# Optimization experiments

Hardware: AMD Instinct MI355X
Metric: run time of the kernel (lower is better)

Reference implementation:

```python
import jax, jax.numpy as jnp
import numpy as np

N = 100000
E = 1600000
HID = 128
NODE_DIM = 128


def _sage_conv(h, src, dst, W_l, b_l, W_r, n_nodes):
    # PyG SAGEConv (mean aggr): out = lin_l(mean_{j in N(i)} h_j) + lin_r(h_i)
    msg = h[src]                                            # [E, d] gather
    s = jax.ops.segment_sum(msg, dst, num_segments=n_nodes)  # [N, d]
    cnt = jax.ops.segment_sum(jnp.ones((msg.shape[0], 1), h.dtype), dst,
                              num_segments=n_nodes)          # [N, 1]
    agg = jnp.where(cnt > 0, s / jnp.maximum(cnt, 1.0), 0.0)
    return agg @ W_l + b_l + h @ W_r


def setup_inputs() -> dict:
    key = jax.random.key(0)
    ks = jax.random.split(key, 12)
    sc = 0.05
    return {
        "pos": jax.random.normal(ks[0], (N, 3), jnp.float32),
        "atomic_number": jax.random.randint(ks[1], (N,), 0, 10, jnp.int64)
            if jax.config.jax_enable_x64 else jax.random.randint(ks[1], (N,), 0, 10, jnp.int32),
        "edge_index": jax.random.randint(ks[2], (2, E), 0, N, jnp.int32),
        # input_proj: Linear(4, HID) — stored as [in, out]
        "W_in": jax.random.normal(ks[3], (4, HID), jnp.float32) * sc,
        "b_in": jnp.zeros((HID,), jnp.float32),
        # conv1: SAGEConv(HID, HID): lin_l (bias), lin_r (no bias)
        "W1_l": jax.random.normal(ks[4], (HID, HID), jnp.float32) * sc,
        "b1": jnp.zeros((HID,), jnp.float32),
        "W1_r": jax.random.normal(ks[5], (HID, HID), jnp.float32) * sc,
        # conv2
        "W2_l": jax.random.normal(ks[6], (HID, HID), jnp.float32) * sc,
        "b2": jnp.zeros((HID,), jnp.float32),
        "W2_r": jax.random.normal(ks[7], (HID, HID), jnp.float32) * sc,
        # out: Linear(HID, NODE_DIM)
        "W_out": jax.random.normal(ks[8], (HID, NODE_DIM), jnp.float32) * sc,
        "b_out": jnp.zeros((NODE_DIM,), jnp.float32),
    }


def reference(pos, atomic_number, edge_index, W_in, b_in, W1_l, b1, W1_r,
              W2_l, b2, W2_r, W_out, b_out):
    src, dst = edge_index[0], edge_index[1]
    z_atom = (atomic_number.astype(pos.dtype) / 10.0)[:, None]   # [N, 1]
    x = jnp.concatenate([z_atom, pos], axis=-1)                   # [N, 4]
    h = jax.nn.relu(x @ W_in + b_in)
    h = jax.nn.relu(_sage_conv(h, src, dst, W1_l, b1, W1_r, h.shape[0]))
    h = jax.nn.relu(_sage_conv(h, src, dst, W2_l, b2, W2_r, h.shape[0]))
    node_states = h @ W_out + b_out                               # [N, node_dim]
    return node_states.mean(axis=0), node_states
```

## Files before the change

### kernel.cpp

```cpp
#include <hip/hip_runtime.h>

#define HID 128
#define BK_SHIFT 9
#define BK_NODES 512
#define BKCAP 10240
#define EDGES_PER_BLKA 8192

typedef _Float16 half_t;
typedef __attribute__((ext_vector_type(8))) _Float16 half8;
typedef __attribute__((ext_vector_type(4))) _Float16 half4;
typedef __attribute__((ext_vector_type(4))) float f32x4;

__global__ __launch_bounds__(256) void k_init(int* __restrict__ bcur,
                                              float* __restrict__ outmean) {
  int i = threadIdx.x;
  bcur[i] = i * BKCAP;
  if (i < HID) outmean[i] = 0.f;
}

__global__ __launch_bounds__(256) void k_packW5(const float* __restrict__ w0,
                                                const float* __restrict__ w1,
                                                const float* __restrict__ w2,
                                                const float* __restrict__ w3,
                                                const float* __restrict__ w4,
                                                half_t* __restrict__ o0,
                                                half_t* __restrict__ o1,
                                                half_t* __restrict__ o2,
                                                half_t* __restrict__ o3,
                                                half_t* __restrict__ o4) {
  int m = blockIdx.x >> 3;
  const float* W = (m == 0) ? w0 : (m == 1) ? w1 : (m == 2) ? w2 : (m == 3) ? w3 : w4;
  half_t* out = (m == 0) ? o0 : (m == 1) ? o1 : (m == 2) ? o2 : (m == 3) ? o3 : o4;
  int tid = (blockIdx.x & 7) * 256 + threadIdx.x;
  int lane = tid & 63;
  int frag = tid >> 6;
  int ks = frag >> 3, nt = frag & 7;
  int k0 = ks * 32 + ((lane >> 4) << 3);
  int col = nt * 16 + (lane & 15);
  half8 v;
#pragma unroll
  for (int i = 0; i < 8; ++i) v[i] = (half_t)W[(k0 + i) * HID + col];
  *(half8*)&out[(size_t)tid * 8] = v;
}

__global__ __launch_bounds__(256) void k_embed(const float* __restrict__ pos,
                                               const int* __restrict__ an,
                                               const float* __restrict__ Win,
                                               const float* __restrict__ bin,
                                               half_t* __restrict__ h, int n) {
  int t = blockIdx.x * 256 + threadIdx.x;
  int i = t >> 5, cg = t & 31;
  if (i >= n) return;
  int j0 = cg << 2;
  float z  = (float)an[i] / 10.0f;
  float px = pos[3 * i + 0], py = pos[3 * i + 1], pz = pos[3 * i + 2];
  float4 w0 = *(const float4*)&Win[0 * HID + j0];
  float4 w1 = *(const float4*)&Win[1 * HID + j0];
  float4 w2 = *(const float4*)&Win[2 * HID + j0];
  float4 w3 = *(const float4*)&Win[3 * HID + j0];
  float4 b  = *(const float4*)&bin[j0];
  float4 o;
  o.x = fmaxf(fmaf(z, w0.x, fmaf(px, w1.x, fmaf(py, w2.x, fmaf(pz, w3.x, b.x)))), 0.f);
  o.y = fmaxf(fmaf(z, w0.y, fmaf(px, w1.y, fmaf(py, w2.y, fmaf(pz, w3.y, b.y)))), 0.f);
  o.z = fmaxf(fmaf(z, w0.z, fmaf(px, w1.z, fmaf(py, w2.z, fmaf(pz, w3.z, b.z)))), 0.f);
  o.w = fmaxf(fmaf(z, w0.w, fmaf(px, w1.w, fmaf(py, w2.w, fmaf(pz, w3.w, b.w)))), 0.f);
  half4 ph;
  ph.x = (half_t)o.x; ph.y = (half_t)o.y; ph.z = (half_t)o.z; ph.w = (half_t)o.w;
  *(half4*)&h[(size_t)i * HID + j0] = ph;
}

__global__ __launch_bounds__(1024) void k_bucketA(const int* __restrict__ src,
                                                  const int* __restrict__ dst,
                                                  int* __restrict__ bcur,
                                                  unsigned* __restrict__ ebuf,
                                                  int e) {
  __shared__ int hist[256];
  __shared__ int resv[256];
  int t = threadIdx.x;
  if (t < 256) hist[t] = 0;
  __syncthreads();
  int e0 = blockIdx.x * EDGES_PER_BLKA;
  int myb[8], myr[8];
  unsigned mypk[8];
#pragma unroll
  for (int i = 0; i < 8; ++i) {
    int idx = e0 + i * 1024 + t;
    if (idx < e) {
      int d = dst[idx];
      int s = src[idx];
      int b = d >> BK_SHIFT;
      myb[i] = b;
      myr[i] = atomicAdd(&hist[b], 1);
      mypk[i] = ((unsigned)s << BK_SHIFT) | (unsigned)(d & (BK_NODES - 1));
    } else {
      myb[i] = -1;
    }
  }
  __syncthreads();
  if (t < 256) resv[t] = (hist[t] > 0) ? atomicAdd(&bcur[t], hist[t]) : 0;
  __syncthreads();
#pragma unroll
  for (int i = 0; i < 8; ++i) {
    if (myb[i] >= 0) ebuf[resv[myb[i]] + myr[i]] = mypk[i];
  }
}

__global__ __launch_bounds__(256) void k_bucketB(const unsigned* __restrict__ ebuf,
                                                 const int* __restrict__ bkend,
                                                 int* __restrict__ offs,
                                                 int* __restrict__ offsE,
                                                 int* __restrict__ csr, int n) {
  __shared__ int hist[BK_NODES];
  __shared__ int pscan[256];
  int b = blockIdx.x;
  int n0 = b << BK_SHIFT;
  int t = threadIdx.x;
  int ebeg = b * BKCAP, eend = bkend[b];
  hist[t] = 0; hist[t + 256] = 0;
  __syncthreads();
  for (int idx = ebeg + t; idx < eend; idx += 256) {
    atomicAdd(&hist[ebuf[idx] & (BK_NODES - 1)], 1);
  }
  __syncthreads();
  int h0 = hist[2 * t], h1 = hist[2 * t + 1];
  int ps = h0 + h1;
  pscan[t] = ps;
  __syncthreads();
  for (int d = 1; d < 256; d <<= 1) {
    int u = (t >= d) ? pscan[t - d] : 0;
    __syncthreads();
    pscan[t] += u;
    __syncthreads();
  }
  int base0 = ebeg + (pscan[t] - ps);
  int g0 = n0 + 2 * t, g1 = g0 + 1;
  if (g0 < n) { offs[g0] = base0;      offsE[g0] = base0 + h0; }
  if (g1 < n) { offs[g1] = base0 + h0; offsE[g1] = base0 + h0 + h1; }
  __syncthreads();
  hist[2 * t] = base0;
  hist[2 * t + 1] = base0 + h0;
  __syncthreads();
  for (int idx = ebeg + t; idx < eend; idx += 256) {
    unsigned pk = ebuf[idx];
    int dl = pk & (BK_NODES - 1);
    int slot = atomicAdd(&hist[dl], 1);
    csr[slot] = (int)(pk >> BK_SHIFT);
  }
}

__global__ __launch_bounds__(256) void k_aggmean_f16(const half_t* __restrict__ h,
                                                     const int* __restrict__ csr,
                                                     const int* __restrict__ offs,
                                                     const int* __restrict__ offsE,
                                                     half_t* __restrict__ out, int n) {
  int w = (blockIdx.x * 256 + threadIdx.x) >> 6;
  int lane = threadIdx.x & 63;
  if (w >= n) return;
  int cs = lane & 15, es = lane >> 4;
  int beg = offs[w], end = offsE[w];
  size_t coff = (size_t)(cs * 8);
  float acc[8];
#pragma unroll
  for (int j = 0; j < 8; ++j) acc[j] = 0.f;
  int e = beg;
  for (; e + 16 <= end; e += 16) {
    int s0 = csr[e + es];
    int s1 = csr[e + 4 + es];
    int s2 = csr[e + 8 + es];
    int s3 = csr[e + 12 + es];
    half8 v0 = *(const half8*)&h[(size_t)s0 * HID + coff];
    half8 v1 = *(const half8*)&h[(size_t)s1 * HID + coff];
    half8 v2 = *(const half8*)&h[(size_t)s2 * HID + coff];
    half8 v3 = *(const half8*)&h[(size_t)s3 * HID + coff];
#pragma unroll
    for (int j = 0; j < 8; ++j)
      acc[j] += ((float)v0[j] + (float)v1[j]) + ((float)v2[j] + (float)v3[j]);
  }
  for (; e < end; e += 4) {
    int ee = e + es;
    if (ee < end) {
      int s = csr[ee];
      half8 v = *(const half8*)&h[(size_t)s * HID + coff];
#pragma unroll
      for (int j = 0; j < 8; ++j) acc[j] += (float)v[j];
    }
  }
#pragma unroll
  for (int j = 0; j < 8; ++j) {
    acc[j] += __shfl_xor(acc[j], 16, 64);
    acc[j] += __shfl_xor(acc[j], 32, 64);
  }
  if (es == 0) {
    int c = end - beg;
    float inv = (c > 0) ? 1.0f / (float)c : 0.0f;
    half8 o;
#pragma unroll
    for (int j = 0; j < 8; ++j) o[j] = (half_t)(acc[j] * inv);
    *(half8*)&out[(size_t)w * HID + coff] = o;
  }
}

__global__ __launch_bounds__(256) void k_sage_mfma(const half_t* __restrict__ ha,
                                                   const half_t* __restrict__ hs,
                                                   const half_t* __restrict__ wl,
                                                   const half_t* __restrict__ wr,
                                                   const float* __restrict__ bias,
                                                   half_t* __restrict__ out, int n) {
  int lane = threadIdx.x & 63;
  int wid = threadIdx.x >> 6;
  int row0 = blockIdx.x * 64 + wid * 16;
  if (row0 >= n) return;
  int arow = row0 + (lane & 15);
  int arowc = arow < n ? arow : n - 1;
  size_t abase = (size_t)arowc * HID + ((lane >> 4) << 3);
  const half8* WL = (const half8*)wl;
  const half8* WR = (const half8*)wr;
  f32x4 acc[8];
#pragma unroll
  for (int t = 0; t < 8; ++t) acc[t] = (f32x4){0.f, 0.f, 0.f, 0.f};
#pragma unroll
  for (int ks = 0; ks < 4; ++ks) {
    half8 aD = *(const half8*)&ha[abase + ks * 32];
    half8 aH = *(const half8*)&hs[abase + ks * 32];
    int fb = ks * 8;
#pragma unroll
    for (int nt = 0; nt < 8; ++nt) {
      half8 bl = WL[(size_t)(fb + nt) * 64 + lane];
      half8 br = WR[(size_t)(fb + nt) * 64 + lane];
      acc[nt] = __builtin_amdgcn_mfma_f32_16x16x32_f16(aD, bl, acc[nt], 0, 0, 0);
      acc[nt] = __builtin_amdgcn_mfma_f32_16x16x32_f16(aH, br, acc[nt], 0, 0, 0);
    }
  }
  int rbase = row0 + ((lane >> 4) << 2);
  int cl = lane & 15;
#pragma unroll
  for (int nt = 0; nt < 8; ++nt) {
    int col = nt * 16 + cl;
    float bv = bias[col];
#pragma unroll
    for (int r = 0; r < 4; ++r) {
      int row = rbase + r;
      if (row < n) {
        float v = fmaxf(acc[nt][r] + bv, 0.f);
        out[(size_t)row * HID + col] = (half_t)v;
      }
    }
  }
}

__global__ __launch_bounds__(256) void k_single_mfma(const half_t* __restrict__ hs,
                                                     const half_t* __restrict__ w,
                                                     const float* __restrict__ bias,
                                                     float* __restrict__ out,
                                                     float* __restrict__ part, int n) {
  __shared__ float colsum[HID];
  int tid = threadIdx.x;
  int lane = tid & 63;
  int wid = tid >> 6;
  if (tid < HID) colsum[tid] = 0.f;
  __syncthreads();
  int row0 = blockIdx.x * 64 + wid * 16;
  bool active = row0 < n;
  f32x4 acc[8];
#pragma unroll
  for (int t = 0; t < 8; ++t) acc[t] = (f32x4){0.f, 0.f, 0.f, 0.f};
  if (active) {
    int arow = row0 + (lane & 15);
    int arowc = arow < n ? arow : n - 1;
    size_t abase = (size_t)arowc * HID + ((lane >> 4) << 3);
    const half8* W8 = (const half8*)w;
#pragma unroll
    for (int ks = 0; ks < 4; ++ks) {
      half8 aH = *(const half8*)&hs[abase + ks * 32];
      int fb = ks * 8;
#pragma unroll
      for (int nt = 0; nt < 8; ++nt) {
        half8 b = W8[(size_t)(fb + nt) * 64 + lane];
        acc[nt] = __builtin_amdgcn_mfma_f32_16x16x32_f16(aH, b, acc[nt], 0, 0, 0);
      }
    }
    int rbase = row0 + ((lane >> 4) << 2);
    int cl = lane & 15;
#pragma unroll
    for (int nt = 0; nt < 8; ++nt) {
      int col = nt * 16 + cl;
      float bv = bias[col];
      float csum = 0.f;
#pragma unroll
      for (int r = 0; r < 4; ++r) {
        int row = rbase + r;
        if (row < n) {
          float v = acc[nt][r] + bv;
          out[(size_t)row * HID + col] = v;
          csum += v;
        }
      }
      atomicAdd(&colsum[col], csum);
    }
  }
  __syncthreads();
  if (tid < HID) part[(size_t)blockIdx.x * HID + tid] = colsum[tid];
}

__global__ __launch_bounds__(256) void k_colfinal(const float* __restrict__ part,
                                                  float* __restrict__ outmean,
                                                  int rows, float inv) {
  __shared__ float red[256];
  int t = threadIdx.x;
  int col = t & 127, half = t >> 7;
  int r0 = blockIdx.x * 256;
  float s = 0.f;
  for (int r = half; r < 256; r += 2) {
    int row = r0 + r;
    if (row < rows) s += part[(size_t)row * HID + col];
  }
  red[t] = s;
  __syncthreads();
  if (t < 128) atomicAdd(&outmean[col], (red[t] + red[t + 128]) * inv);
}

extern "C" void kernel_launch(void* const* d_in, const int* in_sizes, int n_in,
                              void* d_out, int out_size, void* d_ws, size_t ws_size,
                              hipStream_t stream) {
  const float* pos  = (const float*)d_in[0];
  const int*   an   = (const int*)d_in[1];
  const int*   ei   = (const int*)d_in[2];
  const float* Win  = (const float*)d_in[3];
  const float* bin  = (const float*)d_in[4];
  const float* W1l  = (const float*)d_in[5];
  const float* b1   = (const float*)d_in[6];
  const float* W1r  = (const float*)d_in[7];
  const float* W2l  = (const float*)d_in[8];
  const float* b2   = (const float*)d_in[9];
  const float* W2r  = (const float*)d_in[10];
  const float* Wout = (const float*)d_in[11];
  const float* bout = (const float*)d_in[12];

  int N = in_sizes[0] / 3;
  int E = in_sizes[2] / 2;
  const int* srcl = ei;
  const int* dstl = ei + E;

  float* outmean = (float*)d_out;
  float* ns      = (float*)d_out + HID;

  char* p = (char*)d_ws;
  auto take = [&](size_t bytes) {
    char* q = p;
    p += (bytes + 255) & ~(size_t)255;
    return q;
  };
  int nbuck = (N + BK_NODES - 1) / BK_NODES;
  half_t*   H0      = (half_t*)take((size_t)N * HID * 2);
  half_t*   H1      = (half_t*)take((size_t)N * HID * 2);
  half_t*   H2      = (half_t*)take((size_t)N * HID * 2);
  half_t*   D       = (half_t*)take((size_t)N * HID * 2);
  int*      offs    = (int*)take((size_t)N * 4);
  int*      offsE   = (int*)take((size_t)N * 4);
  int*      csr     = (int*)take((size_t)nbuck * BKCAP * 4);
  unsigned* ebuf    = (unsigned*)take((size_t)nbuck * BKCAP * 4);
  int*      bcur    = (int*)take((size_t)256 * 4);
  half_t*   pW1l    = (half_t*)take((size_t)16384 * 2);
  half_t*   pW1r    = (half_t*)take((size_t)16384 * 2);
  half_t*   pW2l    = (half_t*)take((size_t)16384 * 2);
  half_t*   pW2r    = (half_t*)take((size_t)16384 * 2);
  half_t*   pWout   = (half_t*)take((size_t)16384 * 2);
  int gSage = (N + 63) / 64;
  float*    colpart = (float*)take((size_t)gSage * HID * 4);

  int gEmbed = (int)(((size_t)N * 32 + 255) / 256);
  int gWave  = (N + 3) / 4;
  int gBktA  = (E + EDGES_PER_BLKA - 1) / EDGES_PER_BLKA;

  k_init<<<1, 256, 0, stream>>>(bcur, outmean);
  k_packW5<<<40, 256, 0, stream>>>(W1l, W1r, W2l, W2r, Wout,
                                   pW1l, pW1r, pW2l, pW2r, pWout);
  k_embed<<<gEmbed, 256, 0, stream>>>(pos, an, Win, bin, H0, N);
  k_bucketA<<<gBktA, 1024, 0, stream>>>(srcl, dstl, bcur, ebuf, E);
  k_bucketB<<<nbuck, 256, 0, stream>>>(ebuf, bcur, offs, offsE, csr, N);

  k_aggmean_f16<<<gWave, 256, 0, stream>>>(H0, csr, offs, offsE, D, N);
  k_sage_mfma<<<gSage, 256, 0, stream>>>(D, H0, pW1l, pW1r, b1, H1, N);
  k_aggmean_f16<<<gWave, 256, 0, stream>>>(H1, csr, offs, offsE, D, N);
  k_sage_mfma<<<gSage, 256, 0, stream>>>(D, H1, pW2l, pW2r, b2, H2, N);
  k_single_mfma<<<gSage, 256, 0, stream>>>(H2, pWout, bout, ns, colpart, N);
  k_colfinal<<<(gSage + 255) / 256, 256, 0, stream>>>(colpart, outmean, gSage, 1.0f / (float)N);
}
```

Measured before the change: 309.3 us.

## Fuse mean aggregation into SAGE MFMA kernel via shared-memory tile

Merges the neighbor-mean gather kernel and the MFMA linear kernel into one kernel per conv layer. Each block aggregates 64 nodes into an LDS tile, then runs the MFMA GEMM directly from LDS, so the intermediate D buffer is never written to or reread from global memory. The gather is also restructured: each 16-lane group now handles one node with 8 edges in flight instead of splitting edges across lane groups. The risk is fewer independent gather loads in flight per wave, plus lower occupancy from the LDS tile.

```diff
diff --git a/kernel.cpp b/kernel.cpp
--- a/kernel.cpp
+++ b/kernel.cpp
@@ -148,90 +148,96 @@
   }
 }
 
-__global__ __launch_bounds__(256) void k_aggmean_f16(const half_t* __restrict__ h,
-                                                     const int* __restrict__ csr,
-                                                     const int* __restrict__ offs,
-                                                     const int* __restrict__ offsE,
-                                                     half_t* __restrict__ out, int n) {
-  int w = (blockIdx.x * 256 + threadIdx.x) >> 6;
-  int lane = threadIdx.x & 63;
-  if (w >= n) return;
-  int cs = lane & 15, es = lane >> 4;
-  int beg = offs[w], end = offsE[w];
-  size_t coff = (size_t)(cs * 8);
-  float acc[8];
-#pragma unroll
-  for (int j = 0; j < 8; ++j) acc[j] = 0.f;
-  int e = beg;
-  for (; e + 16 <= end; e += 16) {
-    int s0 = csr[e + es];
-    int s1 = csr[e + 4 + es];
-    int s2 = csr[e + 8 + es];
-    int s3 = csr[e + 12 + es];
-    half8 v0 = *(const half8*)&h[(size_t)s0 * HID + coff];
-    half8 v1 = *(const half8*)&h[(size_t)s1 * HID + coff];
-    half8 v2 = *(const half8*)&h[(size_t)s2 * HID + coff];
-    half8 v3 = *(const half8*)&h[(size_t)s3 * HID + coff];
-#pragma unroll
-    for (int j = 0; j < 8; ++j)
-      acc[j] += ((float)v0[j] + (float)v1[j]) + ((float)v2[j] + (float)v3[j]);
-  }
-  for (; e < end; e += 4) {
-    int ee = e + es;
-    if (ee < end) {
-      int s = csr[ee];
-      half8 v = *(const half8*)&h[(size_t)s * HID + coff];
-#pragma unroll
-      for (int j = 0; j < 8; ++j) acc[j] += (float)v[j];
-    }
-  }
-#pragma unroll
-  for (int j = 0; j < 8; ++j) {
-    acc[j] += __shfl_xor(acc[j], 16, 64);
-    acc[j] += __shfl_xor(acc[j], 32, 64);
-  }
-  if (es == 0) {
+__global__ __launch_bounds__(256) void k_conv_fused(const half_t* __restrict__ h,
+                                                    const int* __restrict__ csr,
+                                                    const int* __restrict__ offs,
+                                                    const int* __restrict__ offsE,
+                                                    const half_t* __restrict__ wl,
+                                                    const half_t* __restrict__ wr,
+                                                    const float* __restrict__ bias,
+                                                    half_t* __restrict__ out, int n) {
+  __shared__ half_t Ds[64][136];
+  int tid = threadIdx.x;
+  int lane = tid & 63;
+  int wid = tid >> 6;
+  int row0 = blockIdx.x * 64;
+  int gl = lane & 15;
+  int grp = lane >> 4;
+  size_t coff = (size_t)gl * 8;
+
+  for (int rnd = 0; rnd < 4; ++rnd) {
+    int lrow = wid * 16 + rnd * 4 + grp;
+    int nd = row0 + lrow;
+    int beg = 0, end = 0;
+    if (nd < n) { beg = offs[nd]; end = offsE[nd]; }
+    float acc[8];
+#pragma unroll
+    for (int q = 0; q < 8; ++q) acc[q] = 0.f;
+    for (int e = beg; e < end; e += 8) {
+      int last = end - 1;
+      int s0 = csr[(e + 0) <= last ? (e + 0) : last];
+      int s1 = csr[(e + 1) <= last ? (e + 1) : last];
+      int s2 = csr[(e + 2) <= last ? (e + 2) : last];
+      int s3 = csr[(e + 3) <= last ? (e + 3) : last];
+      int s4 = csr[(e + 4) <= last ? (e + 4) : last];
+      int s5 = csr[(e + 5) <= last ? (e + 5) : last];
+      int s6 = csr[(e + 6) <= last ? (e + 6) : last];
+      int s7 = csr[(e + 7) <= last ? (e + 7) : last];
+      half8 v0 = *(const half8*)&h[(size_t)s0 * HID + coff];
+      half8 v1 = *(const half8*)&h[(size_t)s1 * HID + coff];
+      half8 v2 = *(const half8*)&h[(size_t)s2 * HID + coff];
+      half8 v3 = *(const half8*)&h[(size_t)s3 * HID + coff];
+      half8 v4 = *(const half8*)&h[(size_t)s4 * HID + coff];
+      half8 v5 = *(const half8*)&h[(size_t)s5 * HID + coff];
+      half8 v6 = *(const half8*)&h[(size_t)s6 * HID + coff];
+      half8 v7 = *(const half8*)&h[(size_t)s7 * HID + coff];
+      int rem = end - e;
+#pragma unroll
+      for (int q = 0; q < 8; ++q) {
+        float a = (float)v0[q];
+        if (rem > 1) a += (float)v1[q];
+        if (rem > 2) a += (float)v2[q];
+        if (rem > 3) a += (float)v3[q];
+        if (rem > 4) a += (float)v4[q];
+        if (rem > 5) a += (float)v5[q];
+        if (rem > 6) a += (float)v6[q];
+        if (rem > 7) a += (float)v7[q];
+        acc[q] += a;
+      }
+    }
     int c = end - beg;
     float inv = (c > 0) ? 1.0f / (float)c : 0.0f;
     half8 o;
 #pragma unroll
-    for (int j = 0; j < 8; ++j) o[j] = (half_t)(acc[j] * inv);
-    *(half8*)&out[(size_t)w * HID + coff] = o;
-  }
-}
-
-__global__ __launch_bounds__(256) void k_sage_mfma(const half_t* __restrict__ ha,
-                                                   const half_t* __restrict__ hs,
-                                                   const half_t* __restrict__ wl,
-                                                   const half_t* __restrict__ wr,
-                                                   const float* __restrict__ bias,
-                                                   half_t* __restrict__ out, int n) {
-  int lane = threadIdx.x & 63;
-  int wid = threadIdx.x >> 6;
-  int row0 = blockIdx.x * 64 + wid * 16;
-  if (row0 >= n) return;
-  int arow = row0 + (lane & 15);
-  int arowc = arow < n ? arow : n - 1;
-  size_t abase = (size_t)arowc * HID + ((lane >> 4) << 3);
+    for (int q = 0; q < 8; ++q) o[q] = (half_t)(acc[q] * inv);
+    *(half8*)&Ds[lrow][gl * 8] = o;
+  }
+  __syncthreads();
+
+  int lrow16 = wid * 16 + (lane & 15);
+  int hrow = row0 + lrow16;
+  int hrowc = hrow < n ? hrow : n - 1;
+  size_t hbase = (size_t)hrowc * HID + ((lane >> 4) << 3);
+  int acol = ((lane >> 4) << 3);
   const half8* WL = (const half8*)wl;
   const half8* WR = (const half8*)wr;
-  f32x4 acc[8];
-#pragma unroll
-  for (int t = 0; t < 8; ++t) acc[t] = (f32x4){0.f, 0.f, 0.f, 0.f};
+  f32x4 acc2[8];
+#pragma unroll
+  for (int t2 = 0; t2 < 8; ++t2) acc2[t2] = (f32x4){0.f, 0.f, 0.f, 0.f};
 #pragma unroll
   for (int ks = 0; ks < 4; ++ks) {
-    half8 aD = *(const half8*)&ha[abase + ks * 32];
-    half8 aH = *(const half8*)&hs[abase + ks * 32];
+    half8 aD = *(const half8*)&Ds[lrow16][ks * 32 + acol];
+    half8 aH = *(const half8*)&h[hbase + ks * 32];
     int fb = ks * 8;
 #pragma unroll
     for (int nt = 0; nt < 8; ++nt) {
       half8 bl = WL[(size_t)(fb + nt) * 64 + lane];
       half8 br = WR[(size_t)(fb + nt) * 64 + lane];
-      acc[nt] = __builtin_amdgcn_mfma_f32_16x16x32_f16(aD, bl, acc[nt], 0, 0, 0);
-      acc[nt] = __builtin_amdgcn_mfma_f32_16x16x32_f16(aH, br, acc[nt], 0, 0, 0);
-    }
-  }
-  int rbase = row0 + ((lane >> 4) << 2);
+      acc2[nt] = __builtin_amdgcn_mfma_f32_16x16x32_f16(aD, bl, acc2[nt], 0, 0, 0);
+      acc2[nt] = __builtin_amdgcn_mfma_f32_16x16x32_f16(aH, br, acc2[nt], 0, 0, 0);
+    }
+  }
+  int rbase = row0 + wid * 16 + ((lane >> 4) << 2);
   int cl = lane & 15;
 #pragma unroll
   for (int nt = 0; nt < 8; ++nt) {
@@ -241,7 +247,7 @@
     for (int r = 0; r < 4; ++r) {
       int row = rbase + r;
       if (row < n) {
-        float v = fmaxf(acc[nt][r] + bv, 0.f);
+        float v = fmaxf(acc2[nt][r] + bv, 0.f);
         out[(size_t)row * HID + col] = (half_t)v;
       }
     }
@@ -354,7 +360,6 @@
   half_t*   H0      = (half_t*)take((size_t)N * HID * 2);
   half_t*   H1      = (half_t*)take((size_t)N * HID * 2);
   half_t*   H2      = (half_t*)take((size_t)N * HID * 2);
-  half_t*   D       = (half_t*)take((size_t)N * HID * 2);
   int*      offs    = (int*)take((size_t)N * 4);
   int*      offsE   = (int*)take((size_t)N * 4);
   int*      csr     = (int*)take((size_t)nbuck * BKCAP * 4);
@@ -369,7 +374,6 @@
   float*    colpart = (float*)take((size_t)gSage * HID * 4);
 
   int gEmbed = (int)(((size_t)N * 32 + 255) / 256);
-  int gWave  = (N + 3) / 4;
   int gBktA  = (E + EDGES_PER_BLKA - 1) / EDGES_PER_BLKA;
 
   k_init<<<1, 256, 0, stream>>>(bcur, outmean);
@@ -379,10 +383,8 @@
   k_bucketA<<<gBktA, 1024, 0, stream>>>(srcl, dstl, bcur, ebuf, E);
   k_bucketB<<<nbuck, 256, 0, stream>>>(ebuf, bcur, offs, offsE, csr, N);
 
-  k_aggmean_f16<<<gWave, 256, 0, stream>>>(H0, csr, offs, offsE, D, N);
-  k_sage_mfma<<<gSage, 256, 0, stream>>>(D, H0, pW1l, pW1r, b1, H1, N);
-  k_aggmean_f16<<<gWave, 256, 0, stream>>>(H1, csr, offs, offsE, D, N);
-  k_sage_mfma<<<gSage, 256, 0, stream>>>(D, H1, pW2l, pW2r, b2, H2, N);
+  k_conv_fused<<<gSage, 256, 0, stream>>>(H0, csr, offs, offsE, pW1l, pW1r, b1, H1, N);
+  k_conv_fused<<<gSage, 256, 0, stream>>>(H1, csr, offs, offsE, pW2l, pW2r, b2, H2, N);
   k_single_mfma<<<gSage, 256, 0, stream>>>(H2, pWout, bout, ns, colpart, N);
   k_colfinal<<<(gSage + 255) / 256, 256, 0, stream>>>(colpart, outmean, gSage, 1.0f / (float)N);
 }
```

Measured after the change: 322.1 us. 1.04x slower.
